# Optimization experiments

Measured on AMD Instinct MI355X. Metric: run time of the kernel, lower is better.

Reference implementation:

```python
import jax, jax.numpy as jnp
import numpy as np
import math

B, S, D, H, FF, L = 8, 1024, 1024, 8, 4096, 2
DK = D // H
NEG = -1e32
EPS = 1e-5


def _cosine_pe(seq_len, d_model):
    pos = jnp.arange(seq_len, dtype=jnp.float32)[:, None]
    div = jnp.exp(jnp.arange(0, d_model, 2, dtype=jnp.float32) * (-(math.log(10000.0) / d_model)))
    pe = jnp.zeros((seq_len, d_model), dtype=jnp.float32)
    pe = pe.at[:, 0::2].set(jnp.sin(pos * div))
    pe = pe.at[:, 1::2].set(jnp.cos(pos * div))
    return pe


def setup_inputs() -> dict:
    key = jax.random.key(0)
    ks = jax.random.split(key, 12)
    sc = 0.02
    g = lambda k, shape: (jax.random.normal(k, shape, jnp.float32) * sc)
    return {
        "q_embed": jax.random.normal(ks[0], (B, S, D), jnp.float32),
        "qa_embed": jax.random.normal(ks[1], (B, S, D), jnp.float32),
        "pos_emb": _cosine_pe(S, D),
        "Wk": g(ks[2], (L, D, D)), "bk": jnp.zeros((L, D), jnp.float32),
        "Wv": g(ks[3], (L, D, D)), "bv": jnp.zeros((L, D), jnp.float32),
        "Wo": g(ks[4], (L, D, D)), "bo": jnp.zeros((L, D), jnp.float32),
        "ln1_g": jnp.ones((L, D), jnp.float32), "ln1_b": jnp.zeros((L, D), jnp.float32),
        "W1": g(ks[5], (L, FF, D)), "b1": jnp.zeros((L, FF), jnp.float32),
        "W2": g(ks[6], (L, D, FF)), "b2": jnp.zeros((L, D), jnp.float32),
        "ln2_g": jnp.ones((L, D), jnp.float32), "ln2_b": jnp.zeros((L, D), jnp.float32),
    }


def _layernorm(x, g, b):
    m = jnp.mean(x, axis=-1, keepdims=True)
    v = jnp.mean(jnp.square(x - m), axis=-1, keepdims=True)
    return (x - m) * jax.lax.rsqrt(v + EPS) * g + b


def _mha(x, y, Wk, bk, Wv, bv, Wo, bo, allow):
    # kq_same=1: q and k both come from k_linear applied to x (query==key input)
    k = (jnp.einsum('bsd,od->bso', x, Wk) + bk).reshape(B, S, H, DK).transpose(0, 2, 1, 3)
    q = k  # identical projection and identical input
    v = (jnp.einsum('bsd,od->bso', y, Wv) + bv).reshape(B, S, H, DK).transpose(0, 2, 1, 3)
    scores = jnp.einsum('bhqd,bhkd->bhqk', q, k) / math.sqrt(DK)
    scores = jnp.where(allow, scores, NEG)  # masked_fill(mask==0, -1e32)
    attn = jax.nn.softmax(scores, axis=-1)
    attn = attn.at[:, :, 0, :].set(0.0)  # zero_pad: first query row zeroed
    out = jnp.einsum('bhqk,bhkd->bhqd', attn, v)
    out = out.transpose(0, 2, 1, 3).reshape(B, S, D)
    return jnp.einsum('bsd,od->bso', out, Wo) + bo


def reference(q_embed, qa_embed, pos_emb, Wk, bk, Wv, bv, Wo, bo,
              ln1_g, ln1_b, W1, b1, W2, b2, ln2_g, ln2_b):
    x = q_embed + pos_emb[None]
    y = qa_embed + pos_emb[None]
    # strictly-lower-triangular allowed positions (triu(k=0)==0)
    allow = jnp.tril(jnp.ones((S, S), dtype=bool), -1)[None, None]
    for l in range(L):
        q2 = _mha(x, x, y, Wk[l], bk[l], Wv[l], bv[l], Wo[l], bo[l], allow) if False else _mha(x, y, Wk[l], bk[l], Wv[l], bv[l], Wo[l], bo[l], allow)
        x = _layernorm(x + q2, ln1_g[l], ln1_b[l])
        ff = jnp.einsum('bsf,df->bsd', jax.nn.relu(jnp.einsum('bsd,fd->bsf', x, W1[l]) + b1[l]), W2[l]) + b2[l]
        x = _layernorm(x + ff, ln2_g[l], ln2_b[l])
    return x
```

## Files before the change

### kernel.cpp

```cpp
#include <hip/hip_runtime.h>
#include <hip/hip_bf16.h>
#include <cstdint>
#include <cstddef>

#define B_  8
#define S_  1024
#define D_  1024
#define H_  8
#define FF_ 4096
#define L_  2
#define DK_ 128

typedef __bf16 bf16x8 __attribute__((ext_vector_type(8)));
typedef float  f32x4  __attribute__((ext_vector_type(4)));

__device__ __forceinline__ unsigned short f2bf(float f) {
    union { float f; uint32_t u; } v; v.f = f;
    uint32_t r = v.u + 0x7fffu + ((v.u >> 16) & 1u);
    return (unsigned short)(r >> 16);
}
__device__ __forceinline__ float bf2f(unsigned short u) {
    union { uint32_t u; float f; } v; v.u = ((uint32_t)u) << 16; return v.f;
}

__global__ __launch_bounds__(256) void init_xy(
    const float* __restrict__ qe, const float* __restrict__ qa,
    const float* __restrict__ pe,
    float* __restrict__ x32, unsigned short* __restrict__ xb,
    unsigned short* __restrict__ yb)
{
    int i = (blockIdx.x * 256 + threadIdx.x) * 4;
    int pi = i & (S_ * D_ - 1);
    float4 q = *(const float4*)(qe + i);
    float4 a = *(const float4*)(qa + i);
    float4 p = *(const float4*)(pe + pi);
    float x0 = q.x + p.x, x1 = q.y + p.y, x2 = q.z + p.z, x3 = q.w + p.w;
    float y0 = a.x + p.x, y1 = a.y + p.y, y2 = a.z + p.z, y3 = a.w + p.w;
    *(float4*)(x32 + i) = make_float4(x0, x1, x2, x3);
    ushort4 xo; xo.x = f2bf(x0); xo.y = f2bf(x1); xo.z = f2bf(x2); xo.w = f2bf(x3);
    ushort4 yo; yo.x = f2bf(y0); yo.y = f2bf(y1); yo.z = f2bf(y2); yo.w = f2bf(y3);
    *(ushort4*)(xb + i) = xo;
    *(ushort4*)(yb + i) = yo;
}

__global__ __launch_bounds__(256) void cvt_bf16(
    const float* __restrict__ in, unsigned short* __restrict__ out)
{
    int i = (blockIdx.x * 256 + threadIdx.x) * 4;
    float4 f = *(const float4*)(in + i);
    ushort4 o; o.x = f2bf(f.x); o.y = f2bf(f.y); o.z = f2bf(f.z); o.w = f2bf(f.w);
    *(ushort4*)(out + i) = o;
}

template<bool RELU, int OMODE>
__global__ __launch_bounds__(256) void gemm_bt(
    const unsigned short* __restrict__ A, const unsigned short* __restrict__ W,
    const float* __restrict__ bias, void* __restrict__ Cout,
    int M, int N, int K)
{
    __shared__ unsigned short sA[128][64];
    __shared__ unsigned short sW[128][64];

    const int tid  = threadIdx.x;
    const int lane = tid & 63;
    const int w    = tid >> 6;
    const int l16  = lane & 15;
    const int quad = lane >> 4;
    const int m0 = blockIdx.y * 128;
    const int n0 = blockIdx.x * 128;
    const int rw = (w >> 1) * 64;
    const int cw = (w & 1) * 64;

    const int srow   = lane >> 3;
    const int schunk = lane & 7;

    f32x4 acc[4][4] = {};

    for (int k0 = 0; k0 < K; k0 += 64) {
        __syncthreads();
        #pragma unroll
        for (int i = 0; i < 4; ++i) {
            int r0  = w * 32 + i * 8;
            int row = r0 + srow;
            int gc  = schunk ^ (row & 7);
            const unsigned short* ga = A + (size_t)(m0 + row) * K + k0 + gc * 8;
            const unsigned short* gw = W + (size_t)(n0 + row) * K + k0 + gc * 8;
            __builtin_amdgcn_global_load_lds(
                (const __attribute__((address_space(1))) unsigned int*)ga,
                (__attribute__((address_space(3))) unsigned int*)&sA[r0][0], 16, 0, 0);
            __builtin_amdgcn_global_load_lds(
                (const __attribute__((address_space(1))) unsigned int*)gw,
                (__attribute__((address_space(3))) unsigned int*)&sW[r0][0], 16, 0, 0);
        }
        __syncthreads();

        #pragma unroll
        for (int ks = 0; ks < 2; ++ks) {
            bf16x8 af[4], wf[4];
            #pragma unroll
            for (int t = 0; t < 4; ++t) {
                int arow = rw + t * 16 + l16;
                int achk = (ks * 4 + quad) ^ (arow & 7);
                af[t] = *(const bf16x8*)&sA[arow][achk * 8];
                int wrow = cw + t * 16 + l16;
                int wchk = (ks * 4 + quad) ^ (wrow & 7);
                wf[t] = *(const bf16x8*)&sW[wrow][wchk * 8];
            }
            #pragma unroll
            for (int it = 0; it < 4; ++it)
                #pragma unroll
                for (int jt = 0; jt < 4; ++jt)
                    acc[it][jt] = __builtin_amdgcn_mfma_f32_16x16x32_bf16(
                        af[it], wf[jt], acc[it][jt], 0, 0, 0);
        }
    }

    #pragma unroll
    for (int it = 0; it < 4; ++it)
        #pragma unroll
        for (int jt = 0; jt < 4; ++jt) {
            int row = m0 + rw + it * 16 + quad * 4;
            int col = n0 + cw + jt * 16 + l16;
            float bcol = bias[col];
            float v[4];
            #pragma unroll
            for (int r = 0; r < 4; ++r) {
                v[r] = acc[it][jt][r] + bcol;
                if (RELU) v[r] = fmaxf(v[r], 0.0f);
            }
            if (OMODE == 1) {
                #pragma unroll
                for (int r = 0; r < 4; ++r)
                    ((unsigned short*)Cout)[(size_t)(row + r) * N + col] = f2bf(v[r]);
            } else {
                int key = row & (S_ - 1);
                int bb  = row >> 10;
                int hh  = col >> 7, dim = col & (DK_ - 1);
                unsigned short* dst = (unsigned short*)Cout
                    + ((size_t)(bb * H_ + hh) * DK_ + dim) * S_ + key;
                ushort4 o4; o4.x = f2bf(v[0]); o4.y = f2bf(v[1]);
                o4.z = f2bf(v[2]); o4.w = f2bf(v[3]);
                *(ushort4*)dst = o4;
            }
        }
}

__global__ __launch_bounds__(256) void attn_mfma(
    const unsigned short* __restrict__ Kbuf, const unsigned short* __restrict__ Vtbuf,
    unsigned short* __restrict__ Obuf)
{
    __shared__ unsigned short sK[2][64][128];
    __shared__ unsigned short sVt[2][128][64];
    __shared__ unsigned short sP[4][16][72];

    const int tid  = threadIdx.x;
    const int lane = tid & 63;
    const int w    = tid >> 6;
    const int l16  = lane & 15;
    const int quad = lane >> 4;
    const int pa   = blockIdx.x;
    const int bh   = blockIdx.y;
    const int b    = bh >> 3, h = bh & 7;
    const unsigned short* KB  = Kbuf  + ((size_t)b * S_) * D_ + h * DK_;
    const unsigned short* VTB = Vtbuf + (size_t)bh * DK_ * S_;

    const float scale = 0.08838834764831845f;

    auto stage = [&](int kt, int buf) {
        #pragma unroll
        for (int i = 0; i < 4; ++i) {
            int r0  = w * 16 + i * 4;
            int row = r0 + (lane >> 4);
            int c   = (lane & 15) ^ (row & 15);
            const unsigned short* g = KB + (size_t)(kt * 64 + row) * D_ + c * 8;
            __builtin_amdgcn_global_load_lds(
                (const __attribute__((address_space(1))) unsigned int*)g,
                (__attribute__((address_space(3))) unsigned int*)&sK[buf][r0][0], 16, 0, 0);
        }
        #pragma unroll
        for (int i = 0; i < 4; ++i) {
            int r0  = w * 32 + i * 8;
            int row = r0 + (lane >> 3);
            int c   = (lane & 7) ^ (row & 7);
            const unsigned short* g = VTB + (size_t)row * S_ + kt * 64 + c * 8;
            __builtin_amdgcn_global_load_lds(
                (const __attribute__((address_space(1))) unsigned int*)g,
                (__attribute__((address_space(3))) unsigned int*)&sVt[buf][r0][0], 16, 0, 0);
        }
    };

    #pragma unroll
    for (int half = 0; half < 2; ++half) {
        const int qt = half == 0 ? (15 - pa) : pa;
        const int q0 = qt * 64;

        bf16x8 qf[4];
        {
            const unsigned short* qrow = KB + (size_t)(q0 + w * 16 + l16) * D_ + quad * 8;
            #pragma unroll
            for (int ks = 0; ks < 4; ++ks)
                qf[ks] = *(const bf16x8*)(qrow + ks * 32);
        }

        f32x4 Oacc[8] = {};
        float m_run[4] = {-1e30f, -1e30f, -1e30f, -1e30f};
        float l_run[4] = {};

        int cur = 0;
        stage(0, cur);

        for (int kt = 0; kt <= qt; ++kt) {
            __syncthreads();
            if (kt < qt) stage(kt + 1, cur ^ 1);

            f32x4 sacc[4];
            #pragma unroll
            for (int nt = 0; nt < 4; ++nt) {
                f32x4 a = {};
                #pragma unroll
                for (int ks = 0; ks < 4; ++ks) {
                    int kr = nt * 16 + l16;
                    int p  = (ks * 4 + quad) ^ (kr & 15);
                    bf16x8 kf = *(const bf16x8*)&sK[cur][kr][p * 8];
                    a = __builtin_amdgcn_mfma_f32_16x16x32_bf16(qf[ks], kf, a, 0, 0, 0);
                }
                sacc[nt] = a;
            }

            const bool diag = (kt == qt);
            #pragma unroll
            for (int nt = 0; nt < 4; ++nt)
                #pragma unroll
                for (int r = 0; r < 4; ++r) {
                    float v = sacc[nt][r] * scale;
                    if (diag) {
                        int nidx = nt * 16 + l16;
                        int midx = w * 16 + quad * 4 + r;
                        if (nidx >= midx) v = -1e30f;
                    }
                    sacc[nt][r] = v;
                }

            float alpha[4];
            #pragma unroll
            for (int r = 0; r < 4; ++r) {
                float mx = fmaxf(fmaxf(sacc[0][r], sacc[1][r]), fmaxf(sacc[2][r], sacc[3][r]));
                mx = fmaxf(mx, __shfl_xor(mx, 1));
                mx = fmaxf(mx, __shfl_xor(mx, 2));
                mx = fmaxf(mx, __shfl_xor(mx, 4));
                mx = fmaxf(mx, __shfl_xor(mx, 8));
                float mn = fmaxf(m_run[r], mx);
                alpha[r] = __expf(m_run[r] - mn);
                m_run[r] = mn;
            }
            #pragma unroll
            for (int r = 0; r < 4; ++r) {
                float rs = 0.0f;
                #pragma unroll
                for (int nt = 0; nt < 4; ++nt) {
                    float e = __expf(sacc[nt][r] - m_run[r]);
                    sacc[nt][r] = e;
                    rs += e;
                }
                rs += __shfl_xor(rs, 1);
                rs += __shfl_xor(rs, 2);
                rs += __shfl_xor(rs, 4);
                rs += __shfl_xor(rs, 8);
                l_run[r] = l_run[r] * alpha[r] + rs;
            }
            #pragma unroll
            for (int o = 0; o < 8; ++o)
                #pragma unroll
                for (int r = 0; r < 4; ++r)
                    Oacc[o][r] *= alpha[r];

            #pragma unroll
            for (int nt = 0; nt < 4; ++nt)
                #pragma unroll
                for (int r = 0; r < 4; ++r)
                    sP[w][quad * 4 + r][nt * 16 + l16] = f2bf(sacc[nt][r]);

            bf16x8 pf[2];
            #pragma unroll
            for (int ks = 0; ks < 2; ++ks)
                pf[ks] = *(const bf16x8*)&sP[w][l16][ks * 32 + quad * 8];
            #pragma unroll
            for (int nt = 0; nt < 8; ++nt) {
                #pragma unroll
                for (int ks = 0; ks < 2; ++ks) {
                    int vr = nt * 16 + l16;
                    int p  = (ks * 4 + quad) ^ (vr & 7);
                    bf16x8 vf = *(const bf16x8*)&sVt[cur][vr][p * 8];
                    Oacc[nt] = __builtin_amdgcn_mfma_f32_16x16x32_bf16(pf[ks], vf, Oacc[nt], 0, 0, 0);
                }
            }
            cur ^= 1;
        }

        float inv[4];
        #pragma unroll
        for (int r = 0; r < 4; ++r) {
            int m = q0 + w * 16 + quad * 4 + r;
            inv[r] = (l_run[r] > 0.0f && m != 0) ? 1.0f / l_run[r] : 0.0f;
        }
        #pragma unroll
        for (int nt = 0; nt < 8; ++nt)
            #pragma unroll
            for (int r = 0; r < 4; ++r) {
                int m = q0 + w * 16 + quad * 4 + r;
                Obuf[((size_t)b * S_ + m) * D_ + h * DK_ + nt * 16 + l16] =
                    f2bf(Oacc[nt][r] * inv[r]);
            }
    }
}

__global__ __launch_bounds__(256) void ln_res(
    const float* __restrict__ xin, const unsigned short* __restrict__ delta,
    const float* __restrict__ g, const float* __restrict__ bta,
    float* __restrict__ xout, unsigned short* __restrict__ xbout)
{
    __shared__ float red1[4], red2[4];
    const int row = blockIdx.x;
    const int tid = threadIdx.x;
    const int c = tid * 4;
    const float* xr = xin + (size_t)row * D_;
    const unsigned short* dr = delta + (size_t)row * D_;
    float4 xv = *(const float4*)(xr + c);
    ushort4 du = *(const ushort4*)(dr + c);
    float t0 = xv.x + bf2f(du.x), t1 = xv.y + bf2f(du.y);
    float t2 = xv.z + bf2f(du.z), t3 = xv.w + bf2f(du.w);

    float s = t0 + t1 + t2 + t3;
    #pragma unroll
    for (int off = 32; off > 0; off >>= 1) s += __shfl_down(s, off);
    if ((tid & 63) == 0) red1[tid >> 6] = s;
    __syncthreads();
    float mean = (red1[0] + red1[1] + red1[2] + red1[3]) * (1.0f / 1024.0f);

    float e0 = t0 - mean, e1 = t1 - mean, e2 = t2 - mean, e3 = t3 - mean;
    float ss = e0 * e0 + e1 * e1 + e2 * e2 + e3 * e3;
    #pragma unroll
    for (int off = 32; off > 0; off >>= 1) ss += __shfl_down(ss, off);
    if ((tid & 63) == 0) red2[tid >> 6] = ss;
    __syncthreads();
    float var = (red2[0] + red2[1] + red2[2] + red2[3]) * (1.0f / 1024.0f);
    float rstd = rsqrtf(var + 1e-5f);

    float4 gv = *(const float4*)(g + c);
    float4 bv = *(const float4*)(bta + c);
    float o0 = e0 * rstd * gv.x + bv.x;
    float o1 = e1 * rstd * gv.y + bv.y;
    float o2 = e2 * rstd * gv.z + bv.z;
    float o3 = e3 * rstd * gv.w + bv.w;
    *(float4*)(xout + (size_t)row * D_ + c) = make_float4(o0, o1, o2, o3);
    ushort4 ob; ob.x = f2bf(o0); ob.y = f2bf(o1); ob.z = f2bf(o2); ob.w = f2bf(o3);
    *(ushort4*)(xbout + (size_t)row * D_ + c) = ob;
}

extern "C" void kernel_launch(void* const* d_in, const int* in_sizes, int n_in,
                              void* d_out, int out_size, void* d_ws, size_t ws_size,
                              hipStream_t stream)
{
    const float* qe   = (const float*)d_in[0];
    const float* qa   = (const float*)d_in[1];
    const float* pe   = (const float*)d_in[2];
    const float* Wk   = (const float*)d_in[3];
    const float* bk   = (const float*)d_in[4];
    const float* Wv   = (const float*)d_in[5];
    const float* bv   = (const float*)d_in[6];
    const float* Wo   = (const float*)d_in[7];
    const float* bo   = (const float*)d_in[8];
    const float* ln1g = (const float*)d_in[9];
    const float* ln1b = (const float*)d_in[10];
    const float* W1   = (const float*)d_in[11];
    const float* b1   = (const float*)d_in[12];
    const float* W2   = (const float*)d_in[13];
    const float* b2   = (const float*)d_in[14];
    const float* ln2g = (const float*)d_in[15];
    const float* ln2b = (const float*)d_in[16];

    const size_t BSD = (size_t)B_ * S_ * D_;
    const size_t BSF = (size_t)B_ * S_ * FF_;
    const size_t WDD = (size_t)D_ * D_;
    const size_t WFD = (size_t)FF_ * D_;

    char* p = (char*)d_ws;
    auto take = [&](size_t bytes) { char* r = p; p += (bytes + 255) & ~255ULL; return r; };
    float*          x32   = (float*)take(BSD * 4);
    unsigned short* xb    = (unsigned short*)take(BSD * 2);
    unsigned short* yb    = (unsigned short*)take(BSD * 2);
    unsigned short* delta = (unsigned short*)take(BSD * 2);
    char*           uni   = take(BSF * 2);
    unsigned short* Kb    = (unsigned short*)uni;
    unsigned short* Vt    = Kb + BSD;
    unsigned short* attnb = Vt + BSD;
    unsigned short* hb    = (unsigned short*)uni;
    unsigned short* wslot = (unsigned short*)take(WFD * 2);

    init_xy<<<(int)(BSD / 4 / 256), 256, 0, stream>>>(qe, qa, pe, x32, xb, yb);

    const int M = B_ * S_;
    for (int l = 0; l < L_; ++l) {
        cvt_bf16<<<(int)(WDD / 1024), 256, 0, stream>>>(Wk + l * WDD, wslot);
        gemm_bt<false, 1><<<dim3(D_ / 128, M / 128), 256, 0, stream>>>(
            xb, wslot, bk + l * D_, Kb, M, D_, D_);
        cvt_bf16<<<(int)(WDD / 1024), 256, 0, stream>>>(Wv + l * WDD, wslot);
        gemm_bt<false, 2><<<dim3(D_ / 128, M / 128), 256, 0, stream>>>(
            yb, wslot, bv + l * D_, Vt, M, D_, D_);
        attn_mfma<<<dim3(8, B_ * H_), 256, 0, stream>>>(Kb, Vt, attnb);
        cvt_bf16<<<(int)(WDD / 1024), 256, 0, stream>>>(Wo + l * WDD, wslot);
        gemm_bt<false, 1><<<dim3(D_ / 128, M / 128), 256, 0, stream>>>(
            attnb, wslot, bo + l * D_, delta, M, D_, D_);
        ln_res<<<M, 256, 0, stream>>>(x32, delta, ln1g + l * D_, ln1b + l * D_, x32, xb);
        cvt_bf16<<<(int)(WFD / 1024), 256, 0, stream>>>(W1 + l * WFD, wslot);
        gemm_bt<true, 1><<<dim3(FF_ / 128, M / 128), 256, 0, stream>>>(
            xb, wslot, b1 + l * FF_, hb, M, FF_, D_);
        cvt_bf16<<<(int)(WFD / 1024), 256, 0, stream>>>(W2 + l * WFD, wslot);
        gemm_bt<false, 1><<<dim3(D_ / 128, M / 128), 256, 0, stream>>>(
            hb, wslot, b2 + l * D_, delta, M, D_, FF_);
        float* xo = (l == L_ - 1) ? (float*)d_out : x32;
        ln_res<<<M, 256, 0, stream>>>(x32, delta, ln2g + l * D_, ln2b + l * D_, xo, xb);
    }
}
```

Before: 912.3 us.

## Double-buffer GEMM LDS tiles and keep residual stream in bf16 only

```diff
diff --git a/kernel.cpp b/kernel.cpp
--- a/kernel.cpp
+++ b/kernel.cpp
@@ -26,19 +26,17 @@
 __global__ __launch_bounds__(256) void init_xy(
     const float* __restrict__ qe, const float* __restrict__ qa,
     const float* __restrict__ pe,
-    float* __restrict__ x32, unsigned short* __restrict__ xb,
-    unsigned short* __restrict__ yb)
+    unsigned short* __restrict__ xb, unsigned short* __restrict__ yb)
 {
     int i = (blockIdx.x * 256 + threadIdx.x) * 4;
     int pi = i & (S_ * D_ - 1);
     float4 q = *(const float4*)(qe + i);
     float4 a = *(const float4*)(qa + i);
     float4 p = *(const float4*)(pe + pi);
-    float x0 = q.x + p.x, x1 = q.y + p.y, x2 = q.z + p.z, x3 = q.w + p.w;
-    float y0 = a.x + p.x, y1 = a.y + p.y, y2 = a.z + p.z, y3 = a.w + p.w;
-    *(float4*)(x32 + i) = make_float4(x0, x1, x2, x3);
-    ushort4 xo; xo.x = f2bf(x0); xo.y = f2bf(x1); xo.z = f2bf(x2); xo.w = f2bf(x3);
-    ushort4 yo; yo.x = f2bf(y0); yo.y = f2bf(y1); yo.z = f2bf(y2); yo.w = f2bf(y3);
+    ushort4 xo; xo.x = f2bf(q.x + p.x); xo.y = f2bf(q.y + p.y);
+    xo.z = f2bf(q.z + p.z); xo.w = f2bf(q.w + p.w);
+    ushort4 yo; yo.x = f2bf(a.x + p.x); yo.y = f2bf(a.y + p.y);
+    yo.z = f2bf(a.z + p.z); yo.w = f2bf(a.w + p.w);
     *(ushort4*)(xb + i) = xo;
     *(ushort4*)(yb + i) = yo;
 }
@@ -58,8 +56,8 @@
     const float* __restrict__ bias, void* __restrict__ Cout,
     int M, int N, int K)
 {
-    __shared__ unsigned short sA[128][64];
-    __shared__ unsigned short sW[128][64];
+    __shared__ unsigned short sA[2][128][64];
+    __shared__ unsigned short sW[2][128][64];
 
     const int tid  = threadIdx.x;
     const int lane = tid & 63;
@@ -74,10 +72,7 @@
     const int srow   = lane >> 3;
     const int schunk = lane & 7;
 
-    f32x4 acc[4][4] = {};
-
-    for (int k0 = 0; k0 < K; k0 += 64) {
-        __syncthreads();
+    auto stage = [&](int k0, int buf) {
         #pragma unroll
         for (int i = 0; i < 4; ++i) {
             int r0  = w * 32 + i * 8;
@@ -87,12 +82,21 @@
             const unsigned short* gw = W + (size_t)(n0 + row) * K + k0 + gc * 8;
             __builtin_amdgcn_global_load_lds(
                 (const __attribute__((address_space(1))) unsigned int*)ga,
-                (__attribute__((address_space(3))) unsigned int*)&sA[r0][0], 16, 0, 0);
+                (__attribute__((address_space(3))) unsigned int*)&sA[buf][r0][0], 16, 0, 0);
             __builtin_amdgcn_global_load_lds(
                 (const __attribute__((address_space(1))) unsigned int*)gw,
-                (__attribute__((address_space(3))) unsigned int*)&sW[r0][0], 16, 0, 0);
-        }
+                (__attribute__((address_space(3))) unsigned int*)&sW[buf][r0][0], 16, 0, 0);
+        }
+    };
+
+    f32x4 acc[4][4] = {};
+    const int NK = K >> 6;
+    int cur = 0;
+    stage(0, 0);
+
+    for (int kt = 0; kt < NK; ++kt) {
         __syncthreads();
+        if (kt + 1 < NK) stage((kt + 1) << 6, cur ^ 1);
 
         #pragma unroll
         for (int ks = 0; ks < 2; ++ks) {
@@ -101,10 +105,10 @@
             for (int t = 0; t < 4; ++t) {
                 int arow = rw + t * 16 + l16;
                 int achk = (ks * 4 + quad) ^ (arow & 7);
-                af[t] = *(const bf16x8*)&sA[arow][achk * 8];
+                af[t] = *(const bf16x8*)&sA[cur][arow][achk * 8];
                 int wrow = cw + t * 16 + l16;
                 int wchk = (ks * 4 + quad) ^ (wrow & 7);
-                wf[t] = *(const bf16x8*)&sW[wrow][wchk * 8];
+                wf[t] = *(const bf16x8*)&sW[cur][wrow][wchk * 8];
             }
             #pragma unroll
             for (int it = 0; it < 4; ++it)
@@ -113,6 +117,7 @@
                     acc[it][jt] = __builtin_amdgcn_mfma_f32_16x16x32_bf16(
                         af[it], wf[jt], acc[it][jt], 0, 0, 0);
         }
+        cur ^= 1;
     }
 
     #pragma unroll
@@ -314,21 +319,20 @@
     }
 }
 
+template<bool FINAL>
 __global__ __launch_bounds__(256) void ln_res(
-    const float* __restrict__ xin, const unsigned short* __restrict__ delta,
+    const unsigned short* __restrict__ xin, const unsigned short* __restrict__ delta,
     const float* __restrict__ g, const float* __restrict__ bta,
-    float* __restrict__ xout, unsigned short* __restrict__ xbout)
+    unsigned short* __restrict__ xbout, float* __restrict__ fout)
 {
     __shared__ float red1[4], red2[4];
     const int row = blockIdx.x;
     const int tid = threadIdx.x;
     const int c = tid * 4;
-    const float* xr = xin + (size_t)row * D_;
-    const unsigned short* dr = delta + (size_t)row * D_;
-    float4 xv = *(const float4*)(xr + c);
-    ushort4 du = *(const ushort4*)(dr + c);
-    float t0 = xv.x + bf2f(du.x), t1 = xv.y + bf2f(du.y);
-    float t2 = xv.z + bf2f(du.z), t3 = xv.w + bf2f(du.w);
+    ushort4 xu = *(const ushort4*)(xin + (size_t)row * D_ + c);
+    ushort4 du = *(const ushort4*)(delta + (size_t)row * D_ + c);
+    float t0 = bf2f(xu.x) + bf2f(du.x), t1 = bf2f(xu.y) + bf2f(du.y);
+    float t2 = bf2f(xu.z) + bf2f(du.z), t3 = bf2f(xu.w) + bf2f(du.w);
 
     float s = t0 + t1 + t2 + t3;
     #pragma unroll
@@ -352,9 +356,12 @@
     float o1 = e1 * rstd * gv.y + bv.y;
     float o2 = e2 * rstd * gv.z + bv.z;
     float o3 = e3 * rstd * gv.w + bv.w;
-    *(float4*)(xout + (size_t)row * D_ + c) = make_float4(o0, o1, o2, o3);
-    ushort4 ob; ob.x = f2bf(o0); ob.y = f2bf(o1); ob.z = f2bf(o2); ob.w = f2bf(o3);
-    *(ushort4*)(xbout + (size_t)row * D_ + c) = ob;
+    if (FINAL) {
+        *(float4*)(fout + (size_t)row * D_ + c) = make_float4(o0, o1, o2, o3);
+    } else {
+        ushort4 ob; ob.x = f2bf(o0); ob.y = f2bf(o1); ob.z = f2bf(o2); ob.w = f2bf(o3);
+        *(ushort4*)(xbout + (size_t)row * D_ + c) = ob;
+    }
 }
 
 extern "C" void kernel_launch(void* const* d_in, const int* in_sizes, int n_in,
@@ -386,7 +393,6 @@
 
     char* p = (char*)d_ws;
     auto take = [&](size_t bytes) { char* r = p; p += (bytes + 255) & ~255ULL; return r; };
-    float*          x32   = (float*)take(BSD * 4);
     unsigned short* xb    = (unsigned short*)take(BSD * 2);
     unsigned short* yb    = (unsigned short*)take(BSD * 2);
     unsigned short* delta = (unsigned short*)take(BSD * 2);
@@ -397,7 +403,7 @@
     unsigned short* hb    = (unsigned short*)uni;
     unsigned short* wslot = (unsigned short*)take(WFD * 2);
 
-    init_xy<<<(int)(BSD / 4 / 256), 256, 0, stream>>>(qe, qa, pe, x32, xb, yb);
+    init_xy<<<(int)(BSD / 4 / 256), 256, 0, stream>>>(qe, qa, pe, xb, yb);
 
     const int M = B_ * S_;
     for (int l = 0; l < L_; ++l) {
@@ -411,14 +417,18 @@
         cvt_bf16<<<(int)(WDD / 1024), 256, 0, stream>>>(Wo + l * WDD, wslot);
         gemm_bt<false, 1><<<dim3(D_ / 128, M / 128), 256, 0, stream>>>(
             attnb, wslot, bo + l * D_, delta, M, D_, D_);
-        ln_res<<<M, 256, 0, stream>>>(x32, delta, ln1g + l * D_, ln1b + l * D_, x32, xb);
+        ln_res<false><<<M, 256, 0, stream>>>(xb, delta, ln1g + l * D_, ln1b + l * D_, xb, nullptr);
         cvt_bf16<<<(int)(WFD / 1024), 256, 0, stream>>>(W1 + l * WFD, wslot);
         gemm_bt<true, 1><<<dim3(FF_ / 128, M / 128), 256, 0, stream>>>(
             xb, wslot, b1 + l * FF_, hb, M, FF_, D_);
         cvt_bf16<<<(int)(WFD / 1024), 256, 0, stream>>>(W2 + l * WFD, wslot);
         gemm_bt<false, 1><<<dim3(D_ / 128, M / 128), 256, 0, stream>>>(
             hb, wslot, b2 + l * D_, delta, M, D_, FF_);
-        float* xo = (l == L_ - 1) ? (float*)d_out : x32;
-        ln_res<<<M, 256, 0, stream>>>(x32, delta, ln2g + l * D_, ln2b + l * D_, xo, xb);
+        if (l == L_ - 1)
+            ln_res<true><<<M, 256, 0, stream>>>(xb, delta, ln2g + l * D_, ln2b + l * D_,
+                                               nullptr, (float*)d_out);
+        else
+            ln_res<false><<<M, 256, 0, stream>>>(xb, delta, ln2g + l * D_, ln2b + l * D_,
+                                                xb, nullptr);
     }
 }
```

After: 858.9 us. -5.9%, faster.
